# Optimization experiments

Measured on AMD Instinct MI355X. Metric: run time of the kernel, lower is better.

Reference implementation:

```python
import jax, jax.numpy as jnp
import numpy as np

B = 8
NUM_CLASSES = 80
STRIDES = (8, 16, 32, 64, 128)
HS = (96, 48, 24, 12, 6)
WS = (160, 80, 40, 20, 10)
IMG_H, IMG_W = 768, 1280
OCTAVE_SCALE = 4.0
LOC_THR = 0.01
SCORE_THR = 0.05
IOU_THR = 0.5
NMS_PRE = 1000
MAX_PER_IMG = 100
MAX_RATIO_ANCHOR = abs(float(np.log(1e-6)))        # anchor_coder wh_ratio_clip=1e-6
MAX_RATIO_BBOX = abs(float(np.log(16.0 / 1000.0)))  # bbox_coder default wh_ratio_clip
CLS_OFFSET = 4096.0  # > max image coord, separates classes for class-aware NMS


def setup_inputs():
    inp = {}
    k = 0
    for i, (h, w) in enumerate(zip(HS, WS)):
        for name, c in (("cls_score", NUM_CLASSES), ("bbox_pred", 4), ("shape_pred", 2), ("loc_pred", 1)):
            k += 1
            inp[f"{name}_{i}"] = jax.random.normal(jax.random.fold_in(jax.random.key(0), k), (B, c, h, w), dtype=jnp.float32)
    return inp


def _squares(h, w, stride):
    # mmdet square anchor generator: base size stride*octave_base_scale, ratio 1, center offset 0
    xs = jnp.arange(w, dtype=jnp.float32) * stride
    ys = jnp.arange(h, dtype=jnp.float32) * stride
    yy, xx = jnp.meshgrid(ys, xs, indexing="ij")
    half = 0.5 * OCTAVE_SCALE * stride
    return jnp.stack([xx - half, yy - half, xx + half, yy + half], -1).reshape(-1, 4)


def _delta2bbox(rois, deltas, max_ratio, max_shape=None):
    dx, dy = deltas[..., 0], deltas[..., 1]
    dw = jnp.clip(deltas[..., 2], -max_ratio, max_ratio)
    dh = jnp.clip(deltas[..., 3], -max_ratio, max_ratio)
    px = (rois[..., 0] + rois[..., 2]) * 0.5
    py = (rois[..., 1] + rois[..., 3]) * 0.5
    pw = rois[..., 2] - rois[..., 0]
    ph = rois[..., 3] - rois[..., 1]
    gx = px + pw * dx
    gy = py + ph * dy
    gw = pw * jnp.exp(dw)
    gh = ph * jnp.exp(dh)
    x1, y1 = gx - 0.5 * gw, gy - 0.5 * gh
    x2, y2 = gx + 0.5 * gw, gy + 0.5 * gh
    if max_shape is not None:
        x1 = jnp.clip(x1, 0.0, float(max_shape[1]))
        x2 = jnp.clip(x2, 0.0, float(max_shape[1]))
        y1 = jnp.clip(y1, 0.0, float(max_shape[0]))
        y2 = jnp.clip(y2, 0.0, float(max_shape[0]))
    return jnp.stack([x1, y1, x2, y2], -1)


def _level(cls, bbox, shp, loc, stride, h, w):
    b = cls.shape[0]
    # NOTE: double sigmoid is faithful to the original wrapper (it sigmoids twice)
    scores = jax.nn.sigmoid(jax.nn.sigmoid(jnp.transpose(cls, (0, 2, 3, 1)).reshape(b, -1, NUM_CLASSES)))
    mask = (jax.nn.sigmoid(loc) >= LOC_THR).astype(scores.dtype)
    mask = jnp.transpose(mask, (0, 2, 3, 1)).reshape(b, -1)  # num_anchors == 1
    scores = scores * mask[:, :, None]
    deltas = jnp.transpose(shp, (0, 2, 3, 1)).reshape(b, -1, 2)
    bdel = jnp.concatenate([jnp.zeros_like(deltas), deltas], axis=-1)  # [0,0,dw,dh]
    anchors = _delta2bbox(_squares(h, w, stride)[None], bdel, MAX_RATIO_ANCHOR)  # guided anchors
    bbox = jnp.transpose(bbox, (0, 2, 3, 1)).reshape(b, -1, 4)
    n = scores.shape[1]
    if n < NMS_PRE:  # pad_with_value
        pad = NMS_PRE - n
        scores = jnp.pad(scores, ((0, 0), (0, pad), (0, 0)))
        bbox = jnp.pad(bbox, ((0, 0), (0, pad), (0, 0)))
        anchors = jnp.pad(anchors, ((0, 0), (0, pad), (0, 0)))
    _, idx = jax.lax.top_k(scores.max(-1), NMS_PRE)
    scores = jnp.take_along_axis(scores, idx[:, :, None], axis=1)
    bbox = jnp.take_along_axis(bbox, idx[:, :, None], axis=1)
    anchors = jnp.take_along_axis(anchors, idx[:, :, None], axis=1)
    proposals = _delta2bbox(anchors, bbox, MAX_RATIO_BBOX, (IMG_H, IMG_W))
    return scores, proposals


def _iou_one_vs_all(box, boxes):
    lt = jnp.maximum(box[:2], boxes[:, :2])
    rb = jnp.minimum(box[2:], boxes[:, 2:])
    wh = jnp.clip(rb - lt, 0.0, None)
    inter = wh[:, 0] * wh[:, 1]
    a1 = (box[2] - box[0]) * (box[3] - box[1])
    a2 = (boxes[:, 2] - boxes[:, 0]) * (boxes[:, 3] - boxes[:, 1])
    return inter / (a1 + a2 - inter + 1e-6)


def _nms_single(scores, boxes):
    # class-aware greedy NMS (BatchedNMS semantics): scores [N,C], boxes [N,4]
    n, c = scores.shape
    s = jnp.where(scores > SCORE_THR, scores, 0.0).reshape(-1)  # [N*C]
    offs = (jnp.arange(c, dtype=boxes.dtype) * CLS_OFFSET)[None, :, None]
    cboxes = (boxes[:, None, :] + offs).reshape(-1, 4)  # class-offset boxes

    def step(sv, _):
        i = jnp.argmax(sv)
        sc = sv[i]
        keep = sc > 0.0
        iou = _iou_one_vs_all(cboxes[i], cboxes)
        sv = jnp.where(iou > IOU_THR, 0.0, sv)  # suppresses i itself too
        cls = jnp.where(keep, (i % c).astype(jnp.int32), -1)
        return sv, (boxes[i // c], sc, cls, keep)

    _, (ob, osc, ocls, okeep) = jax.lax.scan(step, s, None, length=MAX_PER_IMG)
    kf = okeep.astype(boxes.dtype)
    return okeep.sum().astype(jnp.int32), ob * kf[:, None], osc * kf, ocls


def _forward(tensors):
    mlvl_scores, mlvl_props = [], []
    for i in range(5):
        s, p = _level(tensors[4 * i], tensors[4 * i + 1], tensors[4 * i + 2], tensors[4 * i + 3],
                      STRIDES[i], HS[i], WS[i])
        mlvl_scores.append(s)
        mlvl_props.append(p)
    scores = jnp.concatenate(mlvl_scores, axis=1)   # [B, 5000, 80]
    props = jnp.concatenate(mlvl_props, axis=1)     # [B, 5000, 4]
    k = min(max(1000, NMS_PRE), scores.shape[1])
    _, idx = jax.lax.top_k(scores.max(-1), k)
    scores = jnp.take_along_axis(scores, idx[:, :, None], axis=1)
    props = jnp.take_along_axis(props, idx[:, :, None], axis=1)
    return jax.vmap(_nms_single)(scores, props)


def reference(cls_score_0, bbox_pred_0, shape_pred_0, loc_pred_0,
              cls_score_1, bbox_pred_1, shape_pred_1, loc_pred_1,
              cls_score_2, bbox_pred_2, shape_pred_2, loc_pred_2,
              cls_score_3, bbox_pred_3, shape_pred_3, loc_pred_3,
              cls_score_4, bbox_pred_4, shape_pred_4, loc_pred_4):
    tensors = [cls_score_0, bbox_pred_0, shape_pred_0, loc_pred_0,
               cls_score_1, bbox_pred_1, shape_pred_1, loc_pred_1,
               cls_score_2, bbox_pred_2, shape_pred_2, loc_pred_2,
               cls_score_3, bbox_pred_3, shape_pred_3, loc_pred_3,
               cls_score_4, bbox_pred_4, shape_pred_4, loc_pred_4]
    num_detected, proposals, out_scores, cls_id = _forward(tensors)
    return num_detected, proposals, out_scores, cls_id
```

## Files before the change

### kernel.cpp

```cpp
#include <hip/hip_runtime.h>
#include <stdint.h>

#define NCLS 80
#define BATCH 8
#define NA 20460
#define TOPK 1000
#define MAXPER 100
#define CAP 8
#define POOL 256
#define IMG_WF 1280.0f
#define IMG_HF 768.0f
#define CLS_OFF 4096.0f
#define MAX_RATIO_ANCHOR 13.815510557964274f
#define MAX_RATIO_BBOX   4.1351665567423557f

#define K2_HALF_UP (0.5 + 0x1p-25)

__constant__ int   c_lvoff[6]  = {0, 15360, 19200, 20160, 20400, 20460};
__constant__ int   c_lvoff4[6] = {0, 3840, 4800, 5040, 5100, 5115};
__constant__ int   c_lw[5]    = {160, 80, 40, 20, 10};
__constant__ int   c_lh[5]    = {96, 48, 24, 12, 6};
__constant__ float c_ls[5]    = {8.f, 16.f, 32.f, 64.f, 128.f};

struct InPtrs {
  const float* cls[5];
  const float* bbox[5];
  const float* shp[5];
  const float* loc[5];
};

__device__ __forceinline__ float sigf(float x) { return 1.0f / (1.0f + expf(-x)); }

__device__ __forceinline__ int wave_red_sum_i32(int v) {
  int t;
  t = __builtin_amdgcn_update_dpp(0, v, 0x111, 0xf, 0xf, false); v += t;
  t = __builtin_amdgcn_update_dpp(0, v, 0x112, 0xf, 0xf, false); v += t;
  t = __builtin_amdgcn_update_dpp(0, v, 0x114, 0xf, 0xf, false); v += t;
  t = __builtin_amdgcn_update_dpp(0, v, 0x118, 0xf, 0xf, false); v += t;
  t = __builtin_amdgcn_update_dpp(0, v, 0x142, 0xf, 0xf, false); v += t;
  t = __builtin_amdgcn_update_dpp(0, v, 0x143, 0xf, 0xf, false); v += t;
  return __builtin_amdgcn_readlane(v, 63);
}
__device__ __forceinline__ void wave_red_top2(unsigned m1, unsigned m2,
                                              unsigned& r1, unsigned& r2) {
#define T2STEP(ctrl) { \
    unsigned o1 = (unsigned)__builtin_amdgcn_update_dpp(0, (int)m1, ctrl, 0xf, 0xf, false); \
    unsigned o2 = (unsigned)__builtin_amdgcn_update_dpp(0, (int)m2, ctrl, 0xf, 0xf, false); \
    unsigned tm = min(m1, o1); \
    m1 = max(m1, o1); \
    m2 = max(tm, max(m2, o2)); }
  T2STEP(0x111) T2STEP(0x112) T2STEP(0x114) T2STEP(0x118) T2STEP(0x142) T2STEP(0x143)
#undef T2STEP
  r1 = (unsigned)__builtin_amdgcn_readlane((int)m1, 63);
  r2 = (unsigned)__builtin_amdgcn_readlane((int)m2, 63);
}

__global__ __launch_bounds__(256) void k_maxscore(InPtrs P, float* maxscore) {
  int gid = blockIdx.x * 256 + threadIdx.x;
  if (gid >= BATCH * (NA / 4)) return;
  int b = gid / (NA / 4);
  int q = gid - b * (NA / 4);
  int l = 0;
  while (q >= c_lvoff4[l + 1]) ++l;
  int hw = c_lh[l] * c_lw[l];
  int sp = (q - c_lvoff4[l]) * 4;
  const float4* cls = (const float4*)(P.cls[l] + (size_t)(b * NCLS) * hw + sp);
  int s4 = hw >> 2;
  float4 m = cls[0];
  for (int c = 1; c < NCLS; ++c) {
    float4 v = cls[(size_t)c * s4];
    m.x = fmaxf(m.x, v.x); m.y = fmaxf(m.y, v.y);
    m.z = fmaxf(m.z, v.z); m.w = fmaxf(m.w, v.w);
  }
  float4 lo = *(const float4*)(P.loc[l] + (size_t)b * hw + sp);
  float4 r;
  r.x = (sigf(lo.x) >= 0.01f) ? sigf(sigf(m.x)) : 0.0f;
  r.y = (sigf(lo.y) >= 0.01f) ? sigf(sigf(m.y)) : 0.0f;
  r.z = (sigf(lo.z) >= 0.01f) ? sigf(sigf(m.z)) : 0.0f;
  r.w = (sigf(lo.w) >= 0.01f) ? sigf(sigf(m.w)) : 0.0f;
  ((float4*)maxscore)[(size_t)b * (NA / 4) + q] = r;
}

__global__ __launch_bounds__(1024) void k_select(const float* maxscore, int* sel) {
  int b = blockIdx.x;
  const unsigned int* ms = (const unsigned int*)(maxscore + (size_t)b * NA);
  int tid = threadIdx.x;
  int wv = tid >> 6;
  int lane = tid & 63;
  __shared__ int s_cnt[2];
  __shared__ int s_pos;
  __shared__ int s_wtot[16];
  __shared__ unsigned long long s_A[1024];
  __shared__ unsigned long long s_B[1024];

  unsigned v[20];
  #pragma unroll
  for (int k = 0; k < 20; ++k) {
    int i = tid + k * 1024;
    v[k] = (i < NA) ? ms[i] : 0u;
  }
  if (tid == 0) { s_cnt[0] = 0; s_cnt[1] = 0; s_pos = 0; }
  __syncthreads();

  int par = 0;
  auto countGE = [&](unsigned mid) -> int {
    int c = 0;
    #pragma unroll
    for (int k = 0; k < 20; ++k) c += (v[k] >= mid) ? 1 : 0;
    c = wave_red_sum_i32(c);
    if (lane == 0) atomicAdd(&s_cnt[par], c);
    if (tid == 0) s_cnt[par ^ 1] = 0;
    __syncthreads();
    int tot = s_cnt[par];
    par ^= 1;
    return tot;
  };

  unsigned lo, hi;
  if (countGE(0x3F000001u) >= TOPK) { lo = 0x3F000001u; hi = 0x3F3C0000u; }
  else                              { lo = 0u;          hi = 1u; }
  while (hi - lo > 1u) {
    unsigned mid = lo + (hi - lo) / 2u;
    if (countGE(mid) >= TOPK) lo = mid; else hi = mid;
  }
  unsigned V = lo;

  if (tid < 1024 - TOPK) s_A[TOPK + tid] = 0ull;
  #pragma unroll
  for (int k = 0; k < 20; ++k) {
    int i = tid + k * 1024;
    bool c = (v[k] > V);
    unsigned long long bal = __ballot(c);
    int base = 0;
    if (lane == 0 && bal) base = atomicAdd(&s_pos, __popcll(bal));
    base = __shfl(base, 0, 64);
    if (c) {
      int off = __popcll(bal & ((1ull << lane) - 1ull));
      s_A[base + off] = ((unsigned long long)v[k] << 32) |
                        (unsigned long long)(0xFFFFFFFFu - (unsigned)i);
    }
  }
  __syncthreads();
  int ngt = s_pos;
  int need = TOPK - ngt;
  const int CH = (NA + 1023) / 1024;
  int i0 = tid * CH, i1 = min(i0 + CH, NA);
  int ceq = 0;
  for (int i = i0; i < i1; ++i) ceq += (ms[i] == V) ? 1 : 0;

  int incl = ceq;
  #pragma unroll
  for (int o = 1; o < 64; o <<= 1) {
    int uu = __shfl_up(incl, o, 64);
    if (lane >= o) incl += uu;
  }
  if (lane == 63) s_wtot[wv] = incl;
  __syncthreads();
  int woff = 0;
  #pragma unroll
  for (int w = 0; w < 16; ++w) woff += (w < wv) ? s_wtot[w] : 0;
  int r = woff + incl - ceq;
  for (int i = i0; i < i1 && r < need; ++i) {
    if (ms[i] == V) {
      s_A[ngt + r] = ((unsigned long long)V << 32) |
                     (unsigned long long)(0xFFFFFFFFu - (unsigned)i);
      ++r;
    }
  }
  __syncthreads();

  unsigned long long key = s_A[tid];
  int tog = 0;
  for (unsigned k = 2; k <= 1024; k <<= 1) {
    for (unsigned j = k >> 1; j > 0; j >>= 1) {
      unsigned long long other;
      if (j >= 64) {
        unsigned long long* cur = tog ? s_A : s_B;
        cur[tid] = key;
        __syncthreads();
        other = cur[tid ^ (int)j];
        tog ^= 1;
      } else {
        other = __shfl_xor(key, (int)j, 64);
      }
      bool takeMax = (((tid & (int)k) == 0) == ((tid & (int)j) == 0));
      unsigned long long mx = (key > other) ? key : other;
      unsigned long long mn = (key > other) ? other : key;
      key = takeMax ? mx : mn;
    }
  }
  if (tid < TOPK) {
    sel[b * TOPK + tid] = (int)(0xFFFFFFFFu - (unsigned)(key & 0xFFFFFFFFull));
  }
}

__global__ __launch_bounds__(256) void k_gather(InPtrs P, const int* sel, float* boxes, float* sv) {
  int wvi = threadIdx.x >> 6;
  int lane = threadIdx.x & 63;
  int wid = blockIdx.x * 4 + wvi;
  int b = wid / TOPK;
  int r = wid - b * TOPK;
  __shared__ float s_sc[4][NCLS];

  int a = sel[b * TOPK + r];
  int l = 0;
  while (a >= c_lvoff[l + 1]) ++l;
  int within = a - c_lvoff[l];
  int W = c_lw[l], H = c_lh[l];
  int y = within / W, x = within - y * W;
  int hw = H * W;
  int sp = within;
  float stride = c_ls[l];
  float px = (float)x * stride;
  float py = (float)y * stride;
  float pw = 4.0f * stride;

  const float* shp = P.shp[l];
  float dws = shp[(b * 2 + 0) * hw + sp];
  float dhs = shp[(b * 2 + 1) * hw + sp];
  dws = fminf(fmaxf(dws, -MAX_RATIO_ANCHOR), MAX_RATIO_ANCHOR);
  dhs = fminf(fmaxf(dhs, -MAX_RATIO_ANCHOR), MAX_RATIO_ANCHOR);
  float gw = pw * expf(dws);
  float gh = pw * expf(dhs);
  float ax1 = px - 0.5f * gw, ax2 = px + 0.5f * gw;
  float ay1 = py - 0.5f * gh, ay2 = py + 0.5f * gh;

  const float* bb = P.bbox[l];
  float dx = bb[(b * 4 + 0) * hw + sp];
  float dy = bb[(b * 4 + 1) * hw + sp];
  float dw = bb[(b * 4 + 2) * hw + sp];
  float dh = bb[(b * 4 + 3) * hw + sp];
  dw = fminf(fmaxf(dw, -MAX_RATIO_BBOX), MAX_RATIO_BBOX);
  dh = fminf(fmaxf(dh, -MAX_RATIO_BBOX), MAX_RATIO_BBOX);
  float px2 = (ax1 + ax2) * 0.5f, py2 = (ay1 + ay2) * 0.5f;
  float pw2 = ax2 - ax1, ph2 = ay2 - ay1;
  float gx = px2 + pw2 * dx, gy = py2 + ph2 * dy;
  float gw2 = pw2 * expf(dw), gh2 = ph2 * expf(dh);
  float x1 = fminf(fmaxf(gx - 0.5f * gw2, 0.0f), IMG_WF);
  float x2 = fminf(fmaxf(gx + 0.5f * gw2, 0.0f), IMG_WF);
  float y1 = fminf(fmaxf(gy - 0.5f * gh2, 0.0f), IMG_HF);
  float y2 = fminf(fmaxf(gy + 0.5f * gh2, 0.0f), IMG_HF);
  if (lane == 0) {
    float4 st; st.x = x1; st.y = y1; st.z = x2; st.w = y2;
    ((float4*)boxes)[b * TOPK + r] = st;
  }

  const float* cls = P.cls[l];
  float sl = sigf(P.loc[l][b * hw + sp]);
  bool mask = (sl >= 0.01f);
  int base = (b * NCLS) * hw + sp;
  for (int c = lane; c < NCLS; c += 64) {
    float vv = 0.0f;
    if (mask) {
      float s2 = sigf(sigf(cls[base + c * hw]));
      vv = (s2 > 0.05f) ? s2 : 0.0f;
    }
    s_sc[wvi][c] = vv;
  }
  __syncthreads();
  int t = threadIdx.x;
  if (t < NCLS) {
    int r0 = blockIdx.x * 4 - b * TOPK;
    float4 o; o.x = s_sc[0][t]; o.y = s_sc[1][t]; o.z = s_sc[2][t]; o.w = s_sc[3][t];
    *(float4*)(sv + ((size_t)(b * NCLS + t) * TOPK + r0)) = o;
  }
}

__global__ __launch_bounds__(256) void k_nms(const float* boxes, const float* sv,
                                             float* keptScore, int* keptRow, int* kc,
                                             const int* flags, const int* gbits, int cap) {
  int bc = blockIdx.x;
  if (flags && flags[bc] == 0) return;
  int b = bc / NCLS;
  int c = bc - b * NCLS;
  int tid = threadIdx.x;
  int wv = tid >> 6, lane = tid & 63;

  unsigned Glow = 0u;
  if (gbits) Glow = ((unsigned)gbits[b]) & 0x3FFFFFu;

  __shared__ float4 s_box[TOPK];
  __shared__ float  s_ard[TOPK];
  __shared__ unsigned long long s_p2[2][4];

  float x1[4], y1[4], x2[4], y2[4], ar[4];
  unsigned key[4];
  float off = (float)c * CLS_OFF;
  const float* svc = sv + (size_t)(b * NCLS + c) * TOPK;
  #pragma unroll
  for (int j = 0; j < 4; ++j) {
    int row = j * 256 + tid;
    if (row < TOPK) {
      float4 bo = ((const float4*)boxes)[b * TOPK + row];
      float a = bo.x + off, d = bo.y + off, e = bo.z + off, f = bo.w + off;
      x1[j] = a; y1[j] = d; x2[j] = e; y2[j] = f;
      ar[j] = (e - a) * (f - d);
      unsigned bits = __float_as_uint(svc[row]);
      key[j] = ((bits & 0x3FFFFFu) << 10) | (1023u - (unsigned)row);
      float sden = ar[j] + 1e-6f;
      bool deg = !((double)ar[j] > (double)sden * K2_HALF_UP);
      float4 sb; sb.x = a; sb.y = d; sb.z = e; sb.w = f;
      s_box[row] = sb;
      s_ard[row] = __uint_as_float(__float_as_uint(ar[j]) | (deg ? 0x80000000u : 0u));
    } else {
      x1[j] = y1[j] = x2[j] = y2[j] = ar[j] = 0.0f;
      key[j] = 0u;
    }
  }
  __syncthreads();

  int kept = 0;
  bool sticky = false;
  float* ks = keptScore + (size_t)(b * NCLS + c) * MAXPER;
  int*   kr = keptRow   + (size_t)(b * NCLS + c) * MAXPER;

  for (int round = 0; round < cap; ++round) {
    int par = round & 1;
    unsigned hi1 = max(key[0], key[1]), lo1 = min(key[0], key[1]);
    unsigned hi2 = max(key[2], key[3]), lo2 = min(key[2], key[3]);
    unsigned m1 = max(hi1, hi2);
    unsigned m2 = max(min(hi1, hi2), max(lo1, lo2));
    unsigned w1, w2;
    wave_red_top2(m1, m2, w1, w2);
    if (lane == 0) s_p2[par][wv] = ((unsigned long long)w1 << 32) | w2;
    __syncthreads();
    unsigned k0 = 0u, k1 = 0u;
    #pragma unroll
    for (int w = 0; w < 4; ++w) {
      unsigned long long pp = s_p2[par][w];
      unsigned p1 = (unsigned)(pp >> 32), p2 = (unsigned)pp;
      unsigned tm = min(k0, p1);
      k0 = max(k0, p1);
      k1 = max(tm, max(k1, p2));
    }
    if (k0 < 1024u) break;
    if ((k0 >> 10) < Glow) break;
    int brow1 = 1023 - (int)(k0 & 1023u);
    float bs1 = __uint_as_float(0x3F000000u | (k0 >> 10));
    float4 bb1 = s_box[brow1];
    unsigned au1 = __float_as_uint(s_ard[brow1]);
    bool deg1 = (au1 >> 31) != 0u;
    float ba1 = __uint_as_float(au1 & 0x7FFFFFFFu);
    if (tid == 0) { ks[kept] = bs1; kr[kept] = brow1; }
    kept++;
    if (deg1) { sticky = true; break; }
    if (kept >= cap) break;
    bool live2 = (k1 >= 1024u) && ((k1 >> 10) >= Glow);
    if (!live2) break;
    bool do2 = false, deg2 = false;
    float4 bb2; float ba2 = 0.0f;
    {
      int brow2 = 1023 - (int)(k1 & 1023u);
      float bs2 = __uint_as_float(0x3F000000u | (k1 >> 10));
      bb2 = s_box[brow2];
      unsigned au2 = __float_as_uint(s_ard[brow2]);
      deg2 = (au2 >> 31) != 0u;
      ba2 = __uint_as_float(au2 & 0x7FFFFFFFu);
      float ltx = fmaxf(bb1.x, bb2.x), rbx = fminf(bb1.z, bb2.z);
      float lty = fmaxf(bb1.y, bb2.y), rby = fminf(bb1.w, bb2.w);
      float w_ = fmaxf(rbx - ltx, 0.0f), h_ = fmaxf(rby - lty, 0.0f);
      float inter = w_ * h_;
      float denom = ((ba1 + ba2) - inter) + 1e-6f;
      if (!((double)inter > (double)denom * K2_HALF_UP)) {
        do2 = true;
        if (tid == 0) { ks[kept] = bs2; kr[kept] = brow2; }
        kept++;
      }
    }
    if (do2 && deg2) { sticky = true; break; }
    #pragma unroll
    for (int j = 0; j < 4; ++j) {
      {
        float ltx = fmaxf(bb1.x, x1[j]), rbx = fminf(bb1.z, x2[j]);
        float lty = fmaxf(bb1.y, y1[j]), rby = fminf(bb1.w, y2[j]);
        float w_ = fmaxf(rbx - ltx, 0.0f), h_ = fmaxf(rby - lty, 0.0f);
        float inter = w_ * h_;
        float denom = ((ba1 + ar[j]) - inter) + 1e-6f;
        if ((double)inter > (double)denom * K2_HALF_UP) key[j] = 0u;
      }
      if (do2) {
        float ltx = fmaxf(bb2.x, x1[j]), rbx = fminf(bb2.z, x2[j]);
        float lty = fmaxf(bb2.y, y1[j]), rby = fminf(bb2.w, y2[j]);
        float w_ = fmaxf(rbx - ltx, 0.0f), h_ = fmaxf(rby - lty, 0.0f);
        float inter = w_ * h_;
        float denom = ((ba2 + ar[j]) - inter) + 1e-6f;
        if ((double)inter > (double)denom * K2_HALF_UP) key[j] = 0u;
      }
    }
    if (kept >= cap) break;
  }
  if (tid == 0) kc[b * NCLS + c] = sticky ? -kept : kept;
}

__global__ __launch_bounds__(256) void k_cut(const float* keptScore, const int* kc,
                                             int* flags, int* gbits) {
  int b = blockIdx.x;
  int tid = threadIdx.x;
  int lane = tid & 63;
  __shared__ int s_abs[NCLS];
  __shared__ int s_neg[NCLS];
  __shared__ int s_cnt[2];

  if (tid < NCLS) {
    int v = kc[b * NCLS + tid];
    s_abs[tid] = (v < 0) ? -v : v;
    s_neg[tid] = (v < 0) ? 1 : 0;
  }
  if (tid == 0) { s_cnt[0] = 0; s_cnt[1] = 0; }
  __syncthreads();

  unsigned vv[3] = {0u, 0u, 0u};
  #pragma unroll
  for (int t = 0; t < 3; ++t) {
    int e = tid + t * 256;
    if (e < NCLS * CAP) {
      int c = e / CAP, k = e - c * CAP;
      if (k < s_abs[c])
        vv[t] = __float_as_uint(keptScore[(size_t)b * NCLS * MAXPER + c * MAXPER + k]);
    }
  }

  int par = 0;
  auto countGE = [&](unsigned mid) -> int {
    int c = ((vv[0] >= mid) ? 1 : 0) + ((vv[1] >= mid) ? 1 : 0) + ((vv[2] >= mid) ? 1 : 0);
    c = wave_red_sum_i32(c);
    if (lane == 0) atomicAdd(&s_cnt[par], c);
    if (tid == 0) s_cnt[par ^ 1] = 0;
    __syncthreads();
    int tot = s_cnt[par];
    par ^= 1;
    return tot;
  };

  unsigned G = 0u;
  if (countGE(0x3F000001u) >= MAXPER) {
    unsigned lo = 0x3F000001u, hi = 0x3F3C0000u;
    while (hi - lo > 1u) {
      unsigned mid = lo + (hi - lo) / 2u;
      if (countGE(mid) >= MAXPER) lo = mid; else hi = mid;
    }
    G = lo;
  }
  if (tid == 0) gbits[b] = (int)G;
  if (tid < NCLS) {
    int f = 0;
    if (s_abs[tid] == CAP && !s_neg[tid]) {
      unsigned slast = __float_as_uint(
          keptScore[(size_t)b * NCLS * MAXPER + tid * MAXPER + (CAP - 1)]);
      if (slast >= G) f = 1;
    }
    flags[b * NCLS + tid] = f;
  }
}

__global__ __launch_bounds__(256) void k_merge(const float* boxes, const float* keptScore,
                                               const int* keptRow, const int* kc, float* out) {
  int b = blockIdx.x;
  int tid = threadIdx.x;
  int wv = tid >> 6, lane = tid & 63;
  __shared__ int s_kc[NCLS];
  __shared__ int s_part[2][4];
  __shared__ int s_pos;
  __shared__ int s_sticky;
  __shared__ int s_navail;
  __shared__ unsigned long long s_pool[POOL];
  __shared__ unsigned long long s_sorted[POOL];

  for (int c = tid; c < NCLS; c += 256) s_kc[c] = kc[b * NCLS + c];
  if (tid == 0) { s_pos = 0; s_sticky = 0x7FFFFFFF; s_navail = 0; }
  for (int i = tid; i < POOL; i += 256) { s_pool[i] = 0ull; s_sorted[i] = 0ull; }
  __syncthreads();

  unsigned sc[32];
  #pragma unroll
  for (int s = 0; s < 32; ++s) {
    int i = tid + s * 256;
    unsigned vv = 0u;
    if (i < NCLS * MAXPER) {
      int c = i / MAXPER, k = i - c * MAXPER;
      int kcv = s_kc[c];
      int ka = (kcv < 0) ? -kcv : kcv;
      if (k < ka) vv = __float_as_uint(keptScore[(size_t)b * NCLS * MAXPER + i]);
    }
    sc[s] = vv;
  }

  int par = 0;
  auto countGE = [&](unsigned mid) -> int {
    int c = 0;
    #pragma unroll
    for (int s = 0; s < 32; ++s) c += (sc[s] >= mid) ? 1 : 0;
    c = wave_red_sum_i32(c);
    if (lane == 0) s_part[par][wv] = c;
    __syncthreads();
    int tot = s_part[par][0] + s_part[par][1] + s_part[par][2] + s_part[par][3];
    par ^= 1;
    return tot;
  };

  int T = countGE(0x3F000001u);
  unsigned V = 0x3F000001u;
  if (T > MAXPER) {
    unsigned lo = 0x3F000001u, hi = 0x3F3C0000u;
    while (hi - lo > 1u) {
      unsigned mid = lo + (hi - lo) / 2u;
      if (countGE(mid) >= MAXPER) lo = mid; else hi = mid;
    }
    V = lo;
  }

  #pragma unroll
  for (int s = 0; s < 32; ++s) {
    if (sc[s] >= V) {
      int i = tid + s * 256;
      int c = i / MAXPER, k = i - c * MAXPER;
      int kcv = s_kc[c];
      int ka = (kcv < 0) ? -kcv : kcv;
      unsigned st = (kcv < 0 && k == ka - 1) ? 1u : 0u;
      unsigned row = (unsigned)keptRow[(size_t)b * NCLS * MAXPER + i];
      unsigned flat = row * 80u + (unsigned)c;
      int p = atomicAdd(&s_pos, 1);
      if (p < POOL)
        s_pool[p] = ((unsigned long long)sc[s] << 32) |
                    (unsigned long long)(0x7FFFFFFFu - ((flat << 1) | st));
    }
  }
  __syncthreads();

  if (tid < POOL) {
    unsigned long long mykey = s_pool[tid];
    if (mykey != 0ull) {
      int rank = 0;
      #pragma unroll 8
      for (int s = 0; s < POOL; ++s) rank += (s_pool[s] > mykey) ? 1 : 0;
      s_sorted[rank] = mykey;
    }
  }
  __syncthreads();

  if (tid < MAXPER) {
    unsigned long long key = s_sorted[tid];
    if (key != 0ull) {
      atomicAdd(&s_navail, 1);
      if ((((unsigned)key) & 1u) == 0u) atomicMin(&s_sticky, tid);
    }
  }
  __syncthreads();
  int navail = s_navail;
  int p = s_sticky;
  int n = (p < navail) ? MAXPER : navail;

  if (tid == 0) out[b] = (float)n;
  const int OB = BATCH;
  const int OP = OB + BATCH * MAXPER * 4;
  const int OS = OP + BATCH * MAXPER;
  if (tid < MAXPER) {
    int k = tid;
    float bx0 = 0.f, bx1 = 0.f, bx2 = 0.f, bx3 = 0.f, scf = 0.f, cf = -1.0f;
    if (k < n) {
      int idx = (k > p) ? p : k;
      unsigned long long key = s_sorted[idx];
      unsigned flat = (0x7FFFFFFFu - (unsigned)key) >> 1;
      unsigned cls = flat % 80u;
      unsigned row = flat / 80u;
      float4 bo = ((const float4*)boxes)[b * TOPK + row];
      bx0 = bo.x; bx1 = bo.y; bx2 = bo.z; bx3 = bo.w;
      scf = __uint_as_float((unsigned)(key >> 32));
      cf = (float)cls;
    }
    float* po = out + OB + (size_t)(b * MAXPER + k) * 4;
    po[0] = bx0; po[1] = bx1; po[2] = bx2; po[3] = bx3;
    out[OP + b * MAXPER + k] = scf;
    out[OS + b * MAXPER + k] = cf;
  }
}

extern "C" void kernel_launch(void* const* d_in, const int* in_sizes, int n_in,
                              void* d_out, int out_size, void* d_ws, size_t ws_size,
                              hipStream_t stream) {
  InPtrs P;
  for (int l = 0; l < 5; ++l) {
    P.cls[l]  = (const float*)d_in[4 * l + 0];
    P.bbox[l] = (const float*)d_in[4 * l + 1];
    P.shp[l]  = (const float*)d_in[4 * l + 2];
    P.loc[l]  = (const float*)d_in[4 * l + 3];
  }
  float* maxscore  = (float*)d_ws;
  int*   sel       = (int*)(maxscore + BATCH * NA);
  float* boxes     = (float*)(sel + BATCH * TOPK);
  float* sv        = boxes + BATCH * TOPK * 4;
  float* keptScore = sv + BATCH * NCLS * TOPK;
  int*   keptRow   = (int*)(keptScore + BATCH * NCLS * MAXPER);
  int*   kc        = keptRow + BATCH * NCLS * MAXPER;
  int*   flags     = kc + BATCH * NCLS;
  int*   gbits     = flags + BATCH * NCLS;
  float* out = (float*)d_out;

  k_maxscore<<<(BATCH * (NA / 4) + 255) / 256, 256, 0, stream>>>(P, maxscore);
  k_select<<<BATCH, 1024, 0, stream>>>(maxscore, sel);
  k_gather<<<BATCH * TOPK / 4, 256, 0, stream>>>(P, sel, boxes, sv);
  k_nms<<<BATCH * NCLS, 256, 0, stream>>>(boxes, sv, keptScore, keptRow, kc,
                                          (const int*)nullptr, (const int*)nullptr, CAP);
  k_cut<<<BATCH, 256, 0, stream>>>(keptScore, kc, flags, gbits);
  k_nms<<<BATCH * NCLS, 256, 0, stream>>>(boxes, sv, keptScore, keptRow, kc,
                                          flags, gbits, MAXPER);
  k_merge<<<BATCH, 256, 0, stream>>>(boxes, keptScore, keptRow, kc, out);
}
```

Before: 224.8 us.

## Replace binary-search threshold in top-k select with two-pass radix histogram

Measured after the change: 213.9 us. -4.9%, faster.

```diff
diff --git a/kernel.cpp b/kernel.cpp
--- a/kernel.cpp
+++ b/kernel.cpp
@@ -87,66 +87,95 @@
   int tid = threadIdx.x;
   int wv = tid >> 6;
   int lane = tid & 63;
-  __shared__ int s_cnt[2];
+  __shared__ unsigned s_h[2048];
+  __shared__ int s_wtot[16];
+  __shared__ int s_res[2];
   __shared__ int s_pos;
-  __shared__ int s_wtot[16];
   __shared__ unsigned long long s_A[1024];
   __shared__ unsigned long long s_B[1024];
 
-  unsigned v[20];
+  unsigned w[20];
+  #pragma unroll
+  for (int k = 0; k < 5; ++k) {
+    int q = tid + k * 1024;
+    uint4 u = (q < NA / 4) ? ((const uint4*)ms)[q] : make_uint4(0u, 0u, 0u, 0u);
+    w[k * 4 + 0] = u.x & 0x3FFFFFu;
+    w[k * 4 + 1] = u.y & 0x3FFFFFu;
+    w[k * 4 + 2] = u.z & 0x3FFFFFu;
+    w[k * 4 + 3] = u.w & 0x3FFFFFu;
+  }
+
+  s_h[tid] = 0u; s_h[tid + 1024] = 0u;
+  if (tid == 0) s_pos = 0;
+  __syncthreads();
+
+  auto scanFind = [&](int target) {
+    int b0 = 2047 - 2 * tid;
+    int h0 = (int)s_h[b0];
+    int h1 = (int)s_h[b0 - 1];
+    int pair = h0 + h1;
+    int incl = pair;
+    #pragma unroll
+    for (int o = 1; o < 64; o <<= 1) {
+      int uu = __shfl_up(incl, o, 64);
+      if (lane >= o) incl += uu;
+    }
+    if (lane == 63) s_wtot[wv] = incl;
+    __syncthreads();
+    int woff = 0;
+    #pragma unroll
+    for (int ww = 0; ww < 16; ++ww) woff += (ww < wv) ? s_wtot[ww] : 0;
+    int excl = woff + incl - pair;
+    if (excl < target && excl + h0 >= target) { s_res[0] = b0; s_res[1] = excl; }
+    int e1 = excl + h0;
+    if (e1 < target && e1 + h1 >= target) { s_res[0] = b0 - 1; s_res[1] = e1; }
+    __syncthreads();
+  };
+
+  #pragma unroll
+  for (int k = 0; k < 20; ++k) atomicAdd(&s_h[w[k] >> 11], 1u);
+  __syncthreads();
+  scanFind(TOPK);
+  int B1 = s_res[0];
+  int NGT1 = s_res[1];
+
+  s_h[tid] = 0u; s_h[tid + 1024] = 0u;
+  __syncthreads();
+  #pragma unroll
+  for (int k = 0; k < 20; ++k)
+    if ((int)(w[k] >> 11) == B1) atomicAdd(&s_h[w[k] & 0x7FFu], 1u);
+  __syncthreads();
+  scanFind(TOPK - NGT1);
+  unsigned V = ((unsigned)B1 << 11) | (unsigned)s_res[0];
+
+  if (tid < 1024 - TOPK) s_A[TOPK + tid] = 0ull;
   #pragma unroll
   for (int k = 0; k < 20; ++k) {
-    int i = tid + k * 1024;
-    v[k] = (i < NA) ? ms[i] : 0u;
-  }
-  if (tid == 0) { s_cnt[0] = 0; s_cnt[1] = 0; s_pos = 0; }
-  __syncthreads();
-
-  int par = 0;
-  auto countGE = [&](unsigned mid) -> int {
-    int c = 0;
-    #pragma unroll
-    for (int k = 0; k < 20; ++k) c += (v[k] >= mid) ? 1 : 0;
-    c = wave_red_sum_i32(c);
-    if (lane == 0) atomicAdd(&s_cnt[par], c);
-    if (tid == 0) s_cnt[par ^ 1] = 0;
-    __syncthreads();
-    int tot = s_cnt[par];
-    par ^= 1;
-    return tot;
-  };
-
-  unsigned lo, hi;
-  if (countGE(0x3F000001u) >= TOPK) { lo = 0x3F000001u; hi = 0x3F3C0000u; }
-  else                              { lo = 0u;          hi = 1u; }
-  while (hi - lo > 1u) {
-    unsigned mid = lo + (hi - lo) / 2u;
-    if (countGE(mid) >= TOPK) lo = mid; else hi = mid;
-  }
-  unsigned V = lo;
-
-  if (tid < 1024 - TOPK) s_A[TOPK + tid] = 0ull;
-  #pragma unroll
-  for (int k = 0; k < 20; ++k) {
-    int i = tid + k * 1024;
-    bool c = (v[k] > V);
+    int i = 4 * (tid + (k >> 2) * 1024) + (k & 3);
+    bool c = (w[k] > V);
     unsigned long long bal = __ballot(c);
     int base = 0;
     if (lane == 0 && bal) base = atomicAdd(&s_pos, __popcll(bal));
     base = __shfl(base, 0, 64);
     if (c) {
       int off = __popcll(bal & ((1ull << lane) - 1ull));
-      s_A[base + off] = ((unsigned long long)v[k] << 32) |
+      s_A[base + off] = ((unsigned long long)w[k] << 32) |
                         (unsigned long long)(0xFFFFFFFFu - (unsigned)i);
     }
   }
   __syncthreads();
   int ngt = s_pos;
   int need = TOPK - ngt;
-  const int CH = (NA + 1023) / 1024;
-  int i0 = tid * CH, i1 = min(i0 + CH, NA);
   int ceq = 0;
-  for (int i = i0; i < i1; ++i) ceq += (ms[i] == V) ? 1 : 0;
+  #pragma unroll
+  for (int k = 0; k < 5; ++k) {
+    int q = tid * 5 + k;
+    if (q < NA / 4) {
+      uint4 u = ((const uint4*)ms)[q];
+      ceq += ((u.x & 0x3FFFFFu) == V ? 1 : 0) + ((u.y & 0x3FFFFFu) == V ? 1 : 0)
+           + ((u.z & 0x3FFFFFu) == V ? 1 : 0) + ((u.w & 0x3FFFFFu) == V ? 1 : 0);
+    }
+  }
 
   int incl = ceq;
   #pragma unroll
@@ -158,10 +187,11 @@
   __syncthreads();
   int woff = 0;
   #pragma unroll
-  for (int w = 0; w < 16; ++w) woff += (w < wv) ? s_wtot[w] : 0;
+  for (int ww = 0; ww < 16; ++ww) woff += (ww < wv) ? s_wtot[ww] : 0;
   int r = woff + incl - ceq;
+  int i0 = tid * 20, i1 = min(i0 + 20, NA);
   for (int i = i0; i < i1 && r < need; ++i) {
-    if (ms[i] == V) {
+    if ((ms[i] & 0x3FFFFFu) == V) {
       s_A[ngt + r] = ((unsigned long long)V << 32) |
                      (unsigned long long)(0xFFFFFFFFu - (unsigned)i);
       ++r;
```
